# Performance work log

Hardware: AMD Instinct MI355X
Metric: run time of the kernel (lower is better)

The kernel has to match this reference:

```python
import jax, jax.numpy as jnp
import numpy as np

B, S, D = 16, 8192, 512
NUM_HEADS = 8
HEAD_DIM = D // NUM_HEADS
SCALE = HEAD_DIM ** -0.5
TEMP = 1.0
THRESHOLD = 0.5
PRIOR = 0.2


def setup_inputs() -> dict:
    key = jax.random.key(0)
    k1, k2, k3, k4 = jax.random.split(key, 4)
    hidden = jax.random.normal(k1, (B, S, D), dtype=jnp.float32)
    lim = float(np.sqrt(6.0 / (D + D)))  # xavier_uniform for square Linear
    Wq = jax.random.uniform(k2, (D, D), minval=-lim, maxval=lim, dtype=jnp.float32)
    Wk = jax.random.uniform(k3, (D, D), minval=-lim, maxval=lim, dtype=jnp.float32)
    noise = jax.random.uniform(k4, (B, S), minval=1e-6, maxval=1.0 - 1e-6, dtype=jnp.float32)
    return {"hidden": hidden, "Wq": Wq, "Wk": Wk, "noise": noise}


def reference(hidden, Wq, Wk, noise):
    # L2-normalize tokens (F.normalize)
    h = hidden / jnp.maximum(jnp.linalg.norm(hidden, axis=-1, keepdims=True), 1e-12)
    Q = h @ Wq.T  # [B,S,D]
    K = h @ Wk.T  # [B,S,D]
    # boundary_scores = (Q K^T * scale).sum(-1) == scale * Q . (sum_j K_j)  (O(n*d) rewrite)
    scores = jnp.einsum('bsd,bd->bs', Q, K.sum(axis=1)) * jnp.float32(SCALE)
    # probs = sigmoid(scores); RelaxedBernoulli logits == scores (clamp is a no-op)
    logistic = jnp.log(noise) - jnp.log1p(-noise)
    soft = jax.nn.sigmoid((scores + logistic) / jnp.float32(TEMP))
    hard = (soft > THRESHOLD).astype(jnp.float32)
    ste = soft + jax.lax.stop_gradient(hard - soft)  # straight-through
    # 'delete' compaction: keep boundary tokens, packed left, zero-padded to S
    keep = hard > 0.0
    order = jnp.argsort(jnp.where(keep, 0, 1), axis=1, stable=True)  # kept indices first, in order
    gathered = jnp.take_along_axis(h * ste[..., None], order[..., None], axis=1)  # [B,S,D]
    counts = keep.sum(axis=1)  # [B]
    valid = jnp.arange(S)[None, :] < counts[:, None]
    pooled = gathered * valid[..., None]
    # Binomial(n=S, p=prior).log_prob(num_boundaries)
    n = jnp.float32(S)
    k = ste.sum(axis=-1)
    p = jnp.float32(PRIOR)
    log_prob = (jax.lax.lgamma(n + 1.0) - jax.lax.lgamma(k + 1.0) - jax.lax.lgamma(n - k + 1.0)
                + k * jnp.log(p) + (n - k) * jnp.log1p(-p))
    loss = -log_prob.mean() / n
    return pooled, loss
```

## Files before the change

### kernel.cpp

```cpp
#include <hip/hip_runtime.h>
#include <math.h>

#define Bn 16
#define Sn 8192
#define Dn 512
#define CHUNKS 64
#define TOK_PER_BLOCK (Sn / CHUNKS)
#define TOK_PER_WAVE (TOK_PER_BLOCK / 4)

__global__ __launch_bounds__(256) void k1_norm_hsum(
    const float* __restrict__ hidden, double* __restrict__ inv_norm,
    double* __restrict__ hsum) {
  __shared__ double lds[Dn];
  const int b = blockIdx.x / CHUNKS;
  const int chunk = blockIdx.x % CHUNKS;
  const int wave = threadIdx.x >> 6;
  const int lane = threadIdx.x & 63;
  for (int i = threadIdx.x; i < Dn; i += 256) lds[i] = 0.0;
  __syncthreads();

  double acc[8] = {0., 0., 0., 0., 0., 0., 0., 0.};
  const int sbase = chunk * TOK_PER_BLOCK + wave * TOK_PER_WAVE;
  for (int t = 0; t < TOK_PER_WAVE; ++t) {
    const int s = sbase + t;
    const size_t tok = (size_t)b * Sn + s;
    const float4* row = (const float4*)(hidden + tok * Dn);
    float4 a = row[lane];
    float4 c = row[64 + lane];
    double ss = (double)a.x * a.x + (double)a.y * a.y + (double)a.z * a.z +
                (double)a.w * a.w + (double)c.x * c.x + (double)c.y * c.y +
                (double)c.z * c.z + (double)c.w * c.w;
#pragma unroll
    for (int m = 32; m >= 1; m >>= 1) ss += __shfl_xor(ss, m, 64);
    double nrm = sqrt(ss);
    if (nrm < 1e-12) nrm = 1e-12;
    const double inv = 1.0 / nrm;
    if (lane == 0) inv_norm[tok] = inv;
    acc[0] += (double)a.x * inv; acc[1] += (double)a.y * inv;
    acc[2] += (double)a.z * inv; acc[3] += (double)a.w * inv;
    acc[4] += (double)c.x * inv; acc[5] += (double)c.y * inv;
    acc[6] += (double)c.z * inv; acc[7] += (double)c.w * inv;
  }
  const int d0 = lane * 4;
  atomicAdd(&lds[d0 + 0], acc[0]);
  atomicAdd(&lds[d0 + 1], acc[1]);
  atomicAdd(&lds[d0 + 2], acc[2]);
  atomicAdd(&lds[d0 + 3], acc[3]);
  atomicAdd(&lds[256 + d0 + 0], acc[4]);
  atomicAdd(&lds[256 + d0 + 1], acc[5]);
  atomicAdd(&lds[256 + d0 + 2], acc[6]);
  atomicAdd(&lds[256 + d0 + 3], acc[7]);
  __syncthreads();
  for (int i = threadIdx.x; i < Dn; i += 256)
    atomicAdd(&hsum[b * Dn + i], lds[i]);
}

__global__ __launch_bounds__(512) void k2_u(
    const float* __restrict__ Wq, const float* __restrict__ Wk,
    const double* __restrict__ hsum, double* __restrict__ u) {
  __shared__ double hl[Dn];
  __shared__ double ks[Dn];
  const int b = blockIdx.x;
  for (int i = threadIdx.x; i < Dn; i += 512) hl[i] = hsum[b * Dn + i];
  __syncthreads();
  const int wave = threadIdx.x >> 6, lane = threadIdx.x & 63;
  for (int dd = 0; dd < 64; ++dd) {
    const int d = wave * 64 + dd;
    double acc = 0.0;
#pragma unroll
    for (int k = 0; k < 8; ++k) {
      const int e = lane + 64 * k;
      acc += (double)Wk[d * Dn + e] * hl[e];
    }
#pragma unroll
    for (int m = 32; m >= 1; m >>= 1) acc += __shfl_xor(acc, m, 64);
    if (lane == 0) ks[d] = acc;
  }
  __syncthreads();
  const int e = threadIdx.x;
  double acc = 0.0;
  for (int d = 0; d < Dn; ++d) acc += (double)Wq[d * Dn + e] * ks[d];
  u[b * Dn + e] = acc;
}

__global__ __launch_bounds__(256) void k3_scores(
    const float* __restrict__ hidden, const double* __restrict__ inv_norm,
    const double* __restrict__ u, const float* __restrict__ noise,
    int* __restrict__ keep) {
  __shared__ double ul[Dn];
  const int b = blockIdx.x / CHUNKS;
  const int chunk = blockIdx.x % CHUNKS;
  for (int i = threadIdx.x; i < Dn; i += 256) ul[i] = u[b * Dn + i];
  __syncthreads();
  const int wave = threadIdx.x >> 6, lane = threadIdx.x & 63;
  const int sbase = chunk * TOK_PER_BLOCK + wave * TOK_PER_WAVE;
  for (int t = 0; t < TOK_PER_WAVE; ++t) {
    const int s = sbase + t;
    const size_t tok = (size_t)b * Sn + s;
    const float4* row = (const float4*)(hidden + tok * Dn);
    float4 a = row[lane], c = row[64 + lane];
    const int d0 = lane * 4;
    double dot = (double)a.x * ul[d0 + 0] + (double)a.y * ul[d0 + 1] +
                 (double)a.z * ul[d0 + 2] + (double)a.w * ul[d0 + 3] +
                 (double)c.x * ul[256 + d0 + 0] + (double)c.y * ul[256 + d0 + 1] +
                 (double)c.z * ul[256 + d0 + 2] + (double)c.w * ul[256 + d0 + 3];
#pragma unroll
    for (int m = 32; m >= 1; m >>= 1) dot += __shfl_xor(dot, m, 64);
    if (lane == 0) {
      double x = 0.125 * inv_norm[tok] * dot;
      const double nv = (double)noise[tok];
      x += log(nv) - log1p(-nv);
      keep[tok] = (x > 0.0) ? 1 : 0;
    }
  }
}

__global__ __launch_bounds__(1024) void k4_scan(
    const int* __restrict__ keep, int* __restrict__ pos,
    int* __restrict__ counts, double* __restrict__ logprob) {
  __shared__ int lds[1024];
  const int b = blockIdx.x, tid = threadIdx.x;
  const size_t base = (size_t)b * Sn + (size_t)tid * 8;
  int v[8], pref[8], tot = 0;
#pragma unroll
  for (int j = 0; j < 8; ++j) {
    v[j] = keep[base + j];
    pref[j] = tot;
    tot += v[j];
  }
  lds[tid] = tot;
  __syncthreads();
  for (int off = 1; off < 1024; off <<= 1) {
    const int val = (tid >= off) ? lds[tid - off] : 0;
    __syncthreads();
    lds[tid] += val;
    __syncthreads();
  }
  const int excl = lds[tid] - tot;
#pragma unroll
  for (int j = 0; j < 8; ++j) pos[base + j] = excl + pref[j];
  if (tid == 1023) {
    const int cnt = lds[1023];
    counts[b] = cnt;
    const double n = (double)Sn, k = (double)cnt;
    logprob[b] = lgamma(n + 1.0) - lgamma(k + 1.0) - lgamma(n - k + 1.0) +
                 k * log(0.2) + (n - k) * log1p(-0.2);
  }
}

__global__ __launch_bounds__(256) void k5_scatter(
    const float* __restrict__ hidden, const double* __restrict__ inv_norm,
    const int* __restrict__ keep, const int* __restrict__ pos,
    const int* __restrict__ counts, const double* __restrict__ logprob,
    float* __restrict__ out) {
  const int b = blockIdx.x / CHUNKS;
  const int chunk = blockIdx.x % CHUNKS;
  const int wave = threadIdx.x >> 6, lane = threadIdx.x & 63;
  const int cnt = counts[b];
  const int sbase = chunk * TOK_PER_BLOCK + wave * TOK_PER_WAVE;
  for (int t = 0; t < TOK_PER_WAVE; ++t) {
    const int s = sbase + t;
    const size_t tok = (size_t)b * Sn + s;
    if (s >= cnt) {
      float4* orow = (float4*)(out + tok * Dn);
      const float4 z = make_float4(0.f, 0.f, 0.f, 0.f);
      orow[lane] = z;
      orow[64 + lane] = z;
    }
    if (keep[tok]) {
      const int p = pos[tok];
      const double inv = inv_norm[tok];
      const float4* row = (const float4*)(hidden + tok * Dn);
      float4 a = row[lane], c = row[64 + lane];
      a.x = (float)((double)a.x * inv); a.y = (float)((double)a.y * inv);
      a.z = (float)((double)a.z * inv); a.w = (float)((double)a.w * inv);
      c.x = (float)((double)c.x * inv); c.y = (float)((double)c.y * inv);
      c.z = (float)((double)c.z * inv); c.w = (float)((double)c.w * inv);
      float4* orow = (float4*)(out + ((size_t)b * Sn + p) * Dn);
      orow[lane] = a;
      orow[64 + lane] = c;
    }
  }
  if (blockIdx.x == 0 && threadIdx.x == 0) {
    double sm = 0.0;
    for (int i = 0; i < Bn; ++i) sm += logprob[i];
    out[(size_t)Bn * Sn * Dn] = (float)(-(sm / (double)Bn) / (double)Sn);
  }
}

extern "C" void kernel_launch(void* const* d_in, const int* in_sizes, int n_in,
                              void* d_out, int out_size, void* d_ws, size_t ws_size,
                              hipStream_t stream) {
  const float* hidden = (const float*)d_in[0];
  const float* Wq = (const float*)d_in[1];
  const float* Wk = (const float*)d_in[2];
  const float* noise = (const float*)d_in[3];
  float* out = (float*)d_out;

  char* ws = (char*)d_ws;
  double* hsum = (double*)(ws);
  double* u = (double*)(ws + 65536);
  double* inv_nrm = (double*)(ws + 131072);
  int* keep = (int*)(ws + 131072 + 1048576);
  int* pos = (int*)(ws + 131072 + 1048576 + 524288);
  int* counts = (int*)(ws + 131072 + 1048576 + 2 * 524288);
  double* logprob = (double*)(ws + 131072 + 1048576 + 2 * 524288 + 256);

  hipMemsetAsync(hsum, 0, Bn * Dn * sizeof(double), stream);

  k1_norm_hsum<<<Bn * CHUNKS, 256, 0, stream>>>(hidden, inv_nrm, hsum);
  k2_u<<<Bn, 512, 0, stream>>>(Wq, Wk, hsum, u);
  k3_scores<<<Bn * CHUNKS, 256, 0, stream>>>(hidden, inv_nrm, u, noise, keep);
  k4_scan<<<Bn, 1024, 0, stream>>>(keep, pos, counts, logprob);
  k5_scatter<<<Bn * CHUNKS, 256, 0, stream>>>(hidden, inv_nrm, keep, pos, counts,
                                              logprob, out);
}
```

Before: 665.1 us.

## Batch four tokens per wave iteration and streamline reductions and scan

The norm/hsum and score kernels now load four token rows per iteration so more memory loads are in flight, and they interleave the four shuffle reductions. k1 replaces the LDS double atomics with per-wave partial buffers summed after the barrier. k2 has each thread compute a full row dot product instead of doing per-row wave reductions. k4 replaces the block-wide LDS Hillis-Steele scan with a wave shuffle scan plus per-wave totals, and uses vectorised int4 loads and stores. These changes add register pressure, and the memory-bound passes over hidden still dominate.

```diff
diff --git a/kernel.cpp b/kernel.cpp
--- a/kernel.cpp
+++ b/kernel.cpp
@@ -8,51 +8,72 @@
 #define TOK_PER_BLOCK (Sn / CHUNKS)
 #define TOK_PER_WAVE (TOK_PER_BLOCK / 4)
 
+__device__ __forceinline__ double dot8sq(const float4& a, const float4& c) {
+  return (double)a.x * a.x + (double)a.y * a.y + (double)a.z * a.z +
+         (double)a.w * a.w + (double)c.x * c.x + (double)c.y * c.y +
+         (double)c.z * c.z + (double)c.w * c.w;
+}
+
 __global__ __launch_bounds__(256) void k1_norm_hsum(
     const float* __restrict__ hidden, double* __restrict__ inv_norm,
     double* __restrict__ hsum) {
-  __shared__ double lds[Dn];
+  __shared__ double part[4][Dn];
   const int b = blockIdx.x / CHUNKS;
   const int chunk = blockIdx.x % CHUNKS;
   const int wave = threadIdx.x >> 6;
   const int lane = threadIdx.x & 63;
-  for (int i = threadIdx.x; i < Dn; i += 256) lds[i] = 0.0;
-  __syncthreads();
 
   double acc[8] = {0., 0., 0., 0., 0., 0., 0., 0.};
   const int sbase = chunk * TOK_PER_BLOCK + wave * TOK_PER_WAVE;
-  for (int t = 0; t < TOK_PER_WAVE; ++t) {
-    const int s = sbase + t;
-    const size_t tok = (size_t)b * Sn + s;
-    const float4* row = (const float4*)(hidden + tok * Dn);
-    float4 a = row[lane];
-    float4 c = row[64 + lane];
-    double ss = (double)a.x * a.x + (double)a.y * a.y + (double)a.z * a.z +
-                (double)a.w * a.w + (double)c.x * c.x + (double)c.y * c.y +
-                (double)c.z * c.z + (double)c.w * c.w;
-#pragma unroll
-    for (int m = 32; m >= 1; m >>= 1) ss += __shfl_xor(ss, m, 64);
-    double nrm = sqrt(ss);
-    if (nrm < 1e-12) nrm = 1e-12;
-    const double inv = 1.0 / nrm;
-    if (lane == 0) inv_norm[tok] = inv;
-    acc[0] += (double)a.x * inv; acc[1] += (double)a.y * inv;
-    acc[2] += (double)a.z * inv; acc[3] += (double)a.w * inv;
-    acc[4] += (double)c.x * inv; acc[5] += (double)c.y * inv;
-    acc[6] += (double)c.z * inv; acc[7] += (double)c.w * inv;
+  const float* hb = hidden + (size_t)b * Sn * Dn;
+
+  for (int t0 = 0; t0 < TOK_PER_WAVE; t0 += 4) {
+    const int s = sbase + t0;
+    const float4* r0 = (const float4*)(hb + (size_t)(s + 0) * Dn);
+    const float4* r1 = (const float4*)(hb + (size_t)(s + 1) * Dn);
+    const float4* r2 = (const float4*)(hb + (size_t)(s + 2) * Dn);
+    const float4* r3 = (const float4*)(hb + (size_t)(s + 3) * Dn);
+    float4 a0 = r0[lane], c0 = r0[64 + lane];
+    float4 a1 = r1[lane], c1 = r1[64 + lane];
+    float4 a2 = r2[lane], c2 = r2[64 + lane];
+    float4 a3 = r3[lane], c3 = r3[64 + lane];
+    double s0 = dot8sq(a0, c0), s1 = dot8sq(a1, c1);
+    double s2 = dot8sq(a2, c2), s3 = dot8sq(a3, c3);
+#pragma unroll
+    for (int m = 32; m >= 1; m >>= 1) {
+      s0 += __shfl_xor(s0, m, 64);
+      s1 += __shfl_xor(s1, m, 64);
+      s2 += __shfl_xor(s2, m, 64);
+      s3 += __shfl_xor(s3, m, 64);
+    }
+    const double i0 = 1.0 / fmax(sqrt(s0), 1e-12);
+    const double i1 = 1.0 / fmax(sqrt(s1), 1e-12);
+    const double i2 = 1.0 / fmax(sqrt(s2), 1e-12);
+    const double i3 = 1.0 / fmax(sqrt(s3), 1e-12);
+    if (lane < 4) {
+      const double iv = (lane == 0) ? i0 : (lane == 1) ? i1 : (lane == 2) ? i2 : i3;
+      inv_norm[(size_t)b * Sn + s + lane] = iv;
+    }
+    acc[0] += (double)a0.x * i0 + (double)a1.x * i1 + (double)a2.x * i2 + (double)a3.x * i3;
+    acc[1] += (double)a0.y * i0 + (double)a1.y * i1 + (double)a2.y * i2 + (double)a3.y * i3;
+    acc[2] += (double)a0.z * i0 + (double)a1.z * i1 + (double)a2.z * i2 + (double)a3.z * i3;
+    acc[3] += (double)a0.w * i0 + (double)a1.w * i1 + (double)a2.w * i2 + (double)a3.w * i3;
+    acc[4] += (double)c0.x * i0 + (double)c1.x * i1 + (double)c2.x * i2 + (double)c3.x * i3;
+    acc[5] += (double)c0.y * i0 + (double)c1.y * i1 + (double)c2.y * i2 + (double)c3.y * i3;
+    acc[6] += (double)c0.z * i0 + (double)c1.z * i1 + (double)c2.z * i2 + (double)c3.z * i3;
+    acc[7] += (double)c0.w * i0 + (double)c1.w * i1 + (double)c2.w * i2 + (double)c3.w * i3;
   }
   const int d0 = lane * 4;
-  atomicAdd(&lds[d0 + 0], acc[0]);
-  atomicAdd(&lds[d0 + 1], acc[1]);
-  atomicAdd(&lds[d0 + 2], acc[2]);
-  atomicAdd(&lds[d0 + 3], acc[3]);
-  atomicAdd(&lds[256 + d0 + 0], acc[4]);
-  atomicAdd(&lds[256 + d0 + 1], acc[5]);
-  atomicAdd(&lds[256 + d0 + 2], acc[6]);
-  atomicAdd(&lds[256 + d0 + 3], acc[7]);
-  __syncthreads();
-  for (int i = threadIdx.x; i < Dn; i += 256)
-    atomicAdd(&hsum[b * Dn + i], lds[i]);
+#pragma unroll
+  for (int k = 0; k < 4; ++k) {
+    part[wave][d0 + k] = acc[k];
+    part[wave][256 + d0 + k] = acc[4 + k];
+  }
+  __syncthreads();
+  for (int i = threadIdx.x; i < Dn; i += 256) {
+    const double v = part[0][i] + part[1][i] + part[2][i] + part[3][i];
+    atomicAdd(&hsum[b * Dn + i], v);
+  }
 }
 
 __global__ __launch_bounds__(512) void k2_u(
@@ -61,26 +82,31 @@
   __shared__ double hl[Dn];
   __shared__ double ks[Dn];
   const int b = blockIdx.x;
-  for (int i = threadIdx.x; i < Dn; i += 512) hl[i] = hsum[b * Dn + i];
-  __syncthreads();
-  const int wave = threadIdx.x >> 6, lane = threadIdx.x & 63;
-  for (int dd = 0; dd < 64; ++dd) {
-    const int d = wave * 64 + dd;
-    double acc = 0.0;
-#pragma unroll
-    for (int k = 0; k < 8; ++k) {
-      const int e = lane + 64 * k;
-      acc += (double)Wk[d * Dn + e] * hl[e];
-    }
-#pragma unroll
-    for (int m = 32; m >= 1; m >>= 1) acc += __shfl_xor(acc, m, 64);
-    if (lane == 0) ks[d] = acc;
-  }
-  __syncthreads();
-  const int e = threadIdx.x;
-  double acc = 0.0;
-  for (int d = 0; d < Dn; ++d) acc += (double)Wq[d * Dn + e] * ks[d];
-  u[b * Dn + e] = acc;
+  const int tid = threadIdx.x;
+  hl[tid] = hsum[b * Dn + tid];
+  __syncthreads();
+  {
+    const float* wrow = Wk + (size_t)tid * Dn;
+    double p0 = 0., p1 = 0., p2 = 0., p3 = 0.;
+    for (int e = 0; e < Dn; e += 4) {
+      p0 += (double)wrow[e + 0] * hl[e + 0];
+      p1 += (double)wrow[e + 1] * hl[e + 1];
+      p2 += (double)wrow[e + 2] * hl[e + 2];
+      p3 += (double)wrow[e + 3] * hl[e + 3];
+    }
+    ks[tid] = (p0 + p1) + (p2 + p3);
+  }
+  __syncthreads();
+  {
+    double p0 = 0., p1 = 0., p2 = 0., p3 = 0.;
+    for (int d = 0; d < Dn; d += 4) {
+      p0 += (double)Wq[(size_t)(d + 0) * Dn + tid] * ks[d + 0];
+      p1 += (double)Wq[(size_t)(d + 1) * Dn + tid] * ks[d + 1];
+      p2 += (double)Wq[(size_t)(d + 2) * Dn + tid] * ks[d + 2];
+      p3 += (double)Wq[(size_t)(d + 3) * Dn + tid] * ks[d + 3];
+    }
+    u[b * Dn + tid] = (p0 + p1) + (p2 + p3);
+  }
 }
 
 __global__ __launch_bounds__(256) void k3_scores(
@@ -93,23 +119,43 @@
   for (int i = threadIdx.x; i < Dn; i += 256) ul[i] = u[b * Dn + i];
   __syncthreads();
   const int wave = threadIdx.x >> 6, lane = threadIdx.x & 63;
+  const int d0 = lane * 4;
+  const double u0 = ul[d0 + 0], u1 = ul[d0 + 1], u2 = ul[d0 + 2], u3 = ul[d0 + 3];
+  const double u4 = ul[256 + d0 + 0], u5 = ul[256 + d0 + 1];
+  const double u6 = ul[256 + d0 + 2], u7 = ul[256 + d0 + 3];
   const int sbase = chunk * TOK_PER_BLOCK + wave * TOK_PER_WAVE;
-  for (int t = 0; t < TOK_PER_WAVE; ++t) {
-    const int s = sbase + t;
-    const size_t tok = (size_t)b * Sn + s;
-    const float4* row = (const float4*)(hidden + tok * Dn);
-    float4 a = row[lane], c = row[64 + lane];
-    const int d0 = lane * 4;
-    double dot = (double)a.x * ul[d0 + 0] + (double)a.y * ul[d0 + 1] +
-                 (double)a.z * ul[d0 + 2] + (double)a.w * ul[d0 + 3] +
-                 (double)c.x * ul[256 + d0 + 0] + (double)c.y * ul[256 + d0 + 1] +
-                 (double)c.z * ul[256 + d0 + 2] + (double)c.w * ul[256 + d0 + 3];
-#pragma unroll
-    for (int m = 32; m >= 1; m >>= 1) dot += __shfl_xor(dot, m, 64);
-    if (lane == 0) {
-      double x = 0.125 * inv_norm[tok] * dot;
+  const float* hb = hidden + (size_t)b * Sn * Dn;
+
+  for (int t0 = 0; t0 < TOK_PER_WAVE; t0 += 4) {
+    const int s = sbase + t0;
+    const float4* r0 = (const float4*)(hb + (size_t)(s + 0) * Dn);
+    const float4* r1 = (const float4*)(hb + (size_t)(s + 1) * Dn);
+    const float4* r2 = (const float4*)(hb + (size_t)(s + 2) * Dn);
+    const float4* r3 = (const float4*)(hb + (size_t)(s + 3) * Dn);
+    float4 a0 = r0[lane], c0 = r0[64 + lane];
+    float4 a1 = r1[lane], c1 = r1[64 + lane];
+    float4 a2 = r2[lane], c2 = r2[64 + lane];
+    float4 a3 = r3[lane], c3 = r3[64 + lane];
+    double d0v = (double)a0.x * u0 + (double)a0.y * u1 + (double)a0.z * u2 + (double)a0.w * u3 +
+                 (double)c0.x * u4 + (double)c0.y * u5 + (double)c0.z * u6 + (double)c0.w * u7;
+    double d1v = (double)a1.x * u0 + (double)a1.y * u1 + (double)a1.z * u2 + (double)a1.w * u3 +
+                 (double)c1.x * u4 + (double)c1.y * u5 + (double)c1.z * u6 + (double)c1.w * u7;
+    double d2v = (double)a2.x * u0 + (double)a2.y * u1 + (double)a2.z * u2 + (double)a2.w * u3 +
+                 (double)c2.x * u4 + (double)c2.y * u5 + (double)c2.z * u6 + (double)c2.w * u7;
+    double d3v = (double)a3.x * u0 + (double)a3.y * u1 + (double)a3.z * u2 + (double)a3.w * u3 +
+                 (double)c3.x * u4 + (double)c3.y * u5 + (double)c3.z * u6 + (double)c3.w * u7;
+#pragma unroll
+    for (int m = 32; m >= 1; m >>= 1) {
+      d0v += __shfl_xor(d0v, m, 64);
+      d1v += __shfl_xor(d1v, m, 64);
+      d2v += __shfl_xor(d2v, m, 64);
+      d3v += __shfl_xor(d3v, m, 64);
+    }
+    if (lane < 4) {
+      const double dj = (lane == 0) ? d0v : (lane == 1) ? d1v : (lane == 2) ? d2v : d3v;
+      const size_t tok = (size_t)b * Sn + s + lane;
       const double nv = (double)noise[tok];
-      x += log(nv) - log1p(-nv);
+      const double x = 0.125 * inv_norm[tok] * dj + log(nv) - log1p(-nv);
       keep[tok] = (x > 0.0) ? 1 : 0;
     }
   }
@@ -118,31 +164,40 @@
 __global__ __launch_bounds__(1024) void k4_scan(
     const int* __restrict__ keep, int* __restrict__ pos,
     int* __restrict__ counts, double* __restrict__ logprob) {
-  __shared__ int lds[1024];
+  __shared__ int wsum[16];
   const int b = blockIdx.x, tid = threadIdx.x;
+  const int lane = tid & 63, wave = tid >> 6;
   const size_t base = (size_t)b * Sn + (size_t)tid * 8;
-  int v[8], pref[8], tot = 0;
+  const int4 kk0 = *(const int4*)(keep + base);
+  const int4 kk1 = *(const int4*)(keep + base + 4);
+  int v[8] = {kk0.x, kk0.y, kk0.z, kk0.w, kk1.x, kk1.y, kk1.z, kk1.w};
+  int pref[8], tot = 0;
 #pragma unroll
   for (int j = 0; j < 8; ++j) {
-    v[j] = keep[base + j];
     pref[j] = tot;
     tot += v[j];
   }
-  lds[tid] = tot;
-  __syncthreads();
-  for (int off = 1; off < 1024; off <<= 1) {
-    const int val = (tid >= off) ? lds[tid - off] : 0;
-    __syncthreads();
-    lds[tid] += val;
-    __syncthreads();
-  }
-  const int excl = lds[tid] - tot;
-#pragma unroll
-  for (int j = 0; j < 8; ++j) pos[base + j] = excl + pref[j];
-  if (tid == 1023) {
-    const int cnt = lds[1023];
-    counts[b] = cnt;
-    const double n = (double)Sn, k = (double)cnt;
+  int x = tot;
+#pragma unroll
+  for (int m = 1; m < 64; m <<= 1) {
+    const int y = __shfl_up(x, m, 64);
+    if (lane >= m) x += y;
+  }
+  if (lane == 63) wsum[wave] = x;
+  __syncthreads();
+  int wp = 0;
+  for (int w = 0; w < wave; ++w) wp += wsum[w];
+  const int excl = wp + x - tot;
+  int4 o0, o1;
+  o0.x = excl + pref[0]; o0.y = excl + pref[1]; o0.z = excl + pref[2]; o0.w = excl + pref[3];
+  o1.x = excl + pref[4]; o1.y = excl + pref[5]; o1.z = excl + pref[6]; o1.w = excl + pref[7];
+  *(int4*)(pos + base) = o0;
+  *(int4*)(pos + base + 4) = o1;
+  if (tid == 0) {
+    int total = 0;
+    for (int w = 0; w < 16; ++w) total += wsum[w];
+    counts[b] = total;
+    const double n = (double)Sn, k = (double)total;
     logprob[b] = lgamma(n + 1.0) - lgamma(k + 1.0) - lgamma(n - k + 1.0) +
                  k * log(0.2) + (n - k) * log1p(-0.2);
   }
@@ -158,11 +213,13 @@
   const int wave = threadIdx.x >> 6, lane = threadIdx.x & 63;
   const int cnt = counts[b];
   const int sbase = chunk * TOK_PER_BLOCK + wave * TOK_PER_WAVE;
+  const float* hb = hidden + (size_t)b * Sn * Dn;
+  float* ob = out + (size_t)b * Sn * Dn;
   for (int t = 0; t < TOK_PER_WAVE; ++t) {
     const int s = sbase + t;
     const size_t tok = (size_t)b * Sn + s;
     if (s >= cnt) {
-      float4* orow = (float4*)(out + tok * Dn);
+      float4* orow = (float4*)(ob + (size_t)s * Dn);
       const float4 z = make_float4(0.f, 0.f, 0.f, 0.f);
       orow[lane] = z;
       orow[64 + lane] = z;
@@ -170,13 +227,13 @@
     if (keep[tok]) {
       const int p = pos[tok];
       const double inv = inv_norm[tok];
-      const float4* row = (const float4*)(hidden + tok * Dn);
+      const float4* row = (const float4*)(hb + (size_t)s * Dn);
       float4 a = row[lane], c = row[64 + lane];
       a.x = (float)((double)a.x * inv); a.y = (float)((double)a.y * inv);
       a.z = (float)((double)a.z * inv); a.w = (float)((double)a.w * inv);
       c.x = (float)((double)c.x * inv); c.y = (float)((double)c.y * inv);
       c.z = (float)((double)c.z * inv); c.w = (float)((double)c.w * inv);
-      float4* orow = (float4*)(out + ((size_t)b * Sn + p) * Dn);
+      float4* orow = (float4*)(ob + (size_t)p * Dn);
       orow[lane] = a;
       orow[64 + lane] = c;
     }
```

Result: faster. 605.5 us (-9.0%).
